# Kernel tuning notes

Measured on AMD Instinct MI355X. Metric: run time of the kernel, lower is better.

The kernel has to match this reference:

```python
import jax, jax.numpy as jnp
import numpy as np

N, C, D = 200000, 100, 256      # samples, classes, dim_out
M = N // C                       # samples per class (y is sorted, equal counts)
K = int(1000 * 0.1)              # num_overlab = int(args.d * args.overlap_ratio)
ALPHA = 1.0                      # args.alpha


def setup_inputs() -> dict:
    key = jax.random.key(0)
    x = jax.random.normal(key, (N, D), dtype=jnp.float32)
    # sorted, balanced labels: class c occupies rows [c*M, (c+1)*M)
    y = jnp.arange(N, dtype=jnp.int32) // M
    return {"x": x, "y": y}


def reference(x, y):
    # per-class means (faithful to get_centers); y is sorted/balanced so a
    # reshape gives the static per-class grouping used below
    xg = x.reshape(C, M, D)                         # [C, M, D]
    centers = jax.ops.segment_sum(x, y, num_segments=C) / M  # [C, D]

    # full center-to-sample L2 distances via ||c||^2 + ||x||^2 - 2 c.x
    x2 = jnp.sum(xg * xg, axis=-1)                  # [C2, M]
    c2 = jnp.sum(centers * centers, axis=-1)        # [C1]
    cx = jnp.einsum('cd,gmd->cgm', centers, xg)     # [C1, C2, M]
    dist = jnp.sqrt(jnp.maximum(c2[:, None, None] + x2[None, :, :] - 2.0 * cx, 0.0))

    # positive: K largest distances from each center to its own samples
    pos = jnp.einsum('iim->im', dist)               # diagonal blocks [C, M]
    pos_mean = jax.lax.top_k(pos, K)[0].mean(axis=1)            # [C]

    # negative: K smallest distances from center c1 to samples of class c2
    neg_mean = (-jax.lax.top_k(-dist, K)[0]).mean(axis=-1)      # [C1, C2]

    lo = jnp.maximum(ALPHA + pos_mean[:, None] - neg_mean, 0.0)  # [C1, C2]
    mask = 1.0 - jnp.eye(C, dtype=lo.dtype)         # skip class_type2 == class_type1
    loss = jnp.sum(lo * mask) / ((C + 1) * (C / 2))
    return loss.reshape(1)
```

## Files before the change

### kernel.cpp

```cpp
#include <hip/hip_runtime.h>
#include <hip/hip_fp16.h>
#include <math.h>

#define N_S 200000
#define C_CLS 100
#define D_DIM 256
#define M_PER 2000
#define K_SEL 100
#define EP_STRIDE 136

typedef __attribute__((ext_vector_type(8))) short short8;
typedef __attribute__((ext_vector_type(4))) float float4v;

__device__ __forceinline__ unsigned int f2bf(float f){
    unsigned int u = __float_as_uint(f);
    u += 0x7FFFu + ((u >> 16) & 1u);
    return u >> 16;
}

__global__ __launch_bounds__(256) void k_sums(const float* __restrict__ x,
                                              float* __restrict__ partial){
    int c = blockIdx.x, s = blockIdx.y;
    int t = threadIdx.x, w = t >> 6, ch = t & 63;
    int rbase = c * M_PER + s * 125;
    float a0 = 0.f, a1 = 0.f, a2 = 0.f, a3 = 0.f;
    for (int i = 0; i < 32; ++i){
        int rl = w + 4 * i;
        if (rl < 125){
            float4v v = *(const float4v*)(x + (size_t)(rbase + rl) * D_DIM + ch * 4);
            a0 += v[0]; a1 += v[1]; a2 += v[2]; a3 += v[3];
        }
    }
    float4v o = {a0, a1, a2, a3};
    *(float4v*)(partial + ((size_t)((c * 16 + s) * 4 + w)) * D_DIM + ch * 4) = o;
}

__global__ __launch_bounds__(256) void k_centers(const float* __restrict__ partial,
                                                 unsigned short* __restrict__ cbf,
                                                 float* __restrict__ c2){
    int c = blockIdx.x, d = threadIdx.x;
    const float* pp = partial + (size_t)c * 64 * D_DIM + d;
    float v = 0.f;
    #pragma unroll
    for (int s = 0; s < 64; ++s) v += pp[(size_t)s * D_DIM];
    v *= (1.0f / (float)M_PER);
    cbf[c * D_DIM + d] = (unsigned short)f2bf(v);
    float sq = v * v;
    #pragma unroll
    for (int m = 1; m < 64; m <<= 1) sq += __shfl_xor(sq, m);
    __shared__ float sred[4];
    if ((threadIdx.x & 63) == 0) sred[threadIdx.x >> 6] = sq;
    __syncthreads();
    if (threadIdx.x == 0) c2[c] = (sred[0] + sred[1]) + (sred[2] + sred[3]);
}

__global__ __launch_bounds__(256, 3) void k_gemm(const float* __restrict__ x,
                                                 const unsigned short* __restrict__ cbf,
                                                 const float* __restrict__ c2,
                                                 _Float16* __restrict__ dist2h){
    __shared__ unsigned short s_cent[C_CLS * 264];
    __shared__ float s_c2[C_CLS];
    int tid = threadIdx.x;
    {
        const uint4* g = (const uint4*)cbf;
        #pragma unroll
        for (int i = 0; i < 13; ++i){
            int q = i * 256 + tid;
            if (q < 3200){
                uint4 v = g[q];
                int row = q >> 5;
                int col = q & 31;
                *(uint4*)((char*)s_cent + row * 528 + col * 16) = v;
            }
        }
        if (tid < C_CLS) s_c2[tid] = c2[tid];
    }
    __syncthreads();

    int wid = tid >> 6, lane = tid & 63, lo = lane & 15, hi = lane >> 4;
    int sbase = blockIdx.x * 128 + wid * 32;
    int j0 = sbase + lo, j1 = sbase + 16 + lo;
    int jr0 = j0 < N_S ? j0 : N_S - 1;
    int jr1 = j1 < N_S ? j1 : N_S - 1;

    float4v acc[7][2];
    #pragma unroll
    for (int a = 0; a < 7; ++a){
        #pragma unroll
        for (int b = 0; b < 2; ++b) acc[a][b] = (float4v){0.f, 0.f, 0.f, 0.f};
    }
    float px2_0 = 0.f, px2_1 = 0.f;

    const float* xr0 = x + (size_t)jr0 * D_DIM + hi * 8;
    const float* xr1 = x + (size_t)jr1 * D_DIM + hi * 8;
    for (int ks = 0; ks < 8; ++ks){
        int k0 = ks * 32;
        float4v v0 = *(const float4v*)(xr0 + k0);
        float4v v1 = *(const float4v*)(xr0 + k0 + 4);
        float4v w0 = *(const float4v*)(xr1 + k0);
        float4v w1 = *(const float4v*)(xr1 + k0 + 4);
        px2_0 += v0[0]*v0[0] + v0[1]*v0[1] + v0[2]*v0[2] + v0[3]*v0[3]
               + v1[0]*v1[0] + v1[1]*v1[1] + v1[2]*v1[2] + v1[3]*v1[3];
        px2_1 += w0[0]*w0[0] + w0[1]*w0[1] + w0[2]*w0[2] + w0[3]*w0[3]
               + w1[0]*w1[0] + w1[1]*w1[1] + w1[2]*w1[2] + w1[3]*w1[3];
        short8 bfr0, bfr1;
        bfr0[0]=(short)f2bf(v0[0]); bfr0[1]=(short)f2bf(v0[1]); bfr0[2]=(short)f2bf(v0[2]); bfr0[3]=(short)f2bf(v0[3]);
        bfr0[4]=(short)f2bf(v1[0]); bfr0[5]=(short)f2bf(v1[1]); bfr0[6]=(short)f2bf(v1[2]); bfr0[7]=(short)f2bf(v1[3]);
        bfr1[0]=(short)f2bf(w0[0]); bfr1[1]=(short)f2bf(w0[1]); bfr1[2]=(short)f2bf(w0[2]); bfr1[3]=(short)f2bf(w0[3]);
        bfr1[4]=(short)f2bf(w1[0]); bfr1[5]=(short)f2bf(w1[1]); bfr1[6]=(short)f2bf(w1[2]); bfr1[7]=(short)f2bf(w1[3]);
        #pragma unroll
        for (int cf = 0; cf < 7; ++cf){
            short8 afr = *(const short8*)((const char*)s_cent + (cf*16 + lo) * 528 + (k0 + hi*8) * 2);
            acc[cf][0] = __builtin_amdgcn_mfma_f32_16x16x32_bf16(afr, bfr0, acc[cf][0], 0, 0, 0);
            acc[cf][1] = __builtin_amdgcn_mfma_f32_16x16x32_bf16(afr, bfr1, acc[cf][1], 0, 0, 0);
        }
    }

    px2_0 += __shfl_xor(px2_0, 16); px2_0 += __shfl_xor(px2_0, 32);
    px2_1 += __shfl_xor(px2_1, 16); px2_1 += __shfl_xor(px2_1, 32);

    __syncthreads();
    _Float16* ep = (_Float16*)s_cent;
    #pragma unroll
    for (int sf = 0; sf < 2; ++sf){
        float x2 = sf ? px2_1 : px2_0;
        int lj = wid * 32 + sf * 16 + lo;
        #pragma unroll
        for (int cf = 0; cf < 7; ++cf){
            #pragma unroll
            for (int r = 0; r < 4; ++r){
                int c1 = cf * 16 + hi * 4 + r;
                if (c1 < C_CLS){
                    float d2 = s_c2[c1] + x2 - 2.0f * acc[cf][sf][r];
                    ep[c1 * EP_STRIDE + lj] = (_Float16)fmaxf(d2, 0.f);
                }
            }
        }
    }
    __syncthreads();

    int blockbase = blockIdx.x * 128;
    int vj = N_S - blockbase; vj = vj > 128 ? 128 : vj;
    for (int q = tid; q < C_CLS * 16; q += 256){
        int row = q >> 4, st = (q & 15) * 8;
        if (st < vj){
            uint4 v = *(const uint4*)(ep + row * EP_STRIDE + st);
            *(uint4*)(dist2h + (size_t)row * N_S + blockbase + st) = v;
        }
    }
}

__global__ __launch_bounds__(256) void k_select(const _Float16* __restrict__ dist2h,
                                                float* __restrict__ pos_mean,
                                                float* __restrict__ neg_mean){
    int lane = threadIdx.x & 63;
    int pair = blockIdx.x * 4 + (threadIdx.x >> 6);
    int c1 = pair / 100, c2 = pair - c1 * 100;
    bool diag = (c1 == c2);
    const uint4* base =
        (const uint4*)(dist2h + (size_t)c1 * N_S + (size_t)c2 * M_PER);

    int keys[32];
    int kmin = 0x10000, kmax = 0;
    #pragma unroll
    for (int i = 0; i < 4; ++i){
        int q = i * 64 + lane;
        if (q < 250){
            uint4 v = base[q];
            unsigned wds[4] = {v.x, v.y, v.z, v.w};
            #pragma unroll
            for (int j = 0; j < 4; ++j){
                int klo = (int)(wds[j] & 0xFFFFu);
                int khi = (int)(wds[j] >> 16);
                if (diag){ klo = 0xFFFF - klo; khi = 0xFFFF - khi; }
                keys[i*8 + 2*j]     = klo;
                keys[i*8 + 2*j + 1] = khi;
                kmin = klo < kmin ? klo : kmin;  kmin = khi < kmin ? khi : kmin;
                kmax = klo > kmax ? klo : kmax;  kmax = khi > kmax ? khi : kmax;
            }
        } else {
            #pragma unroll
            for (int j = 0; j < 8; ++j) keys[i*8 + j] = 0x10000;
        }
    }
    #pragma unroll
    for (int m = 1; m < 64; m <<= 1){
        int a = __shfl_xor(kmin, m); kmin = a < kmin ? a : kmin;
        int b = __shfl_xor(kmax, m); kmax = b > kmax ? b : kmax;
    }

    int lo = kmin, hi = kmax;
    while (lo < hi){
        int mid = (lo + hi) >> 1;
        int c = 0;
        #pragma unroll
        for (int i = 0; i < 32; ++i) c += (keys[i] <= mid) ? 1 : 0;
        #pragma unroll
        for (int m = 1; m < 64; m <<= 1) c += __shfl_xor(c, m);
        if (c >= K_SEL) hi = mid; else lo = mid + 1;
    }
    int t = lo;

    float sb = 0.f;
    int nb = 0;
    #pragma unroll
    for (int i = 0; i < 32; ++i){
        int key = keys[i];
        if (key < t){
            unsigned short u = (unsigned short)(diag ? (0xFFFF - key) : key);
            sb += sqrtf(__half2float(__ushort_as_half(u)));
            nb++;
        }
    }
    #pragma unroll
    for (int m = 1; m < 64; m <<= 1){
        sb += __shfl_xor(sb, m);
        nb += __shfl_xor(nb, m);
    }
    if (lane == 0){
        unsigned short ut = (unsigned short)(diag ? (0xFFFF - t) : t);
        float tval = sqrtf(__half2float(__ushort_as_half(ut)));
        int need = K_SEL - nb;
        float mean = (sb + (float)need * tval) * (1.0f / (float)K_SEL);
        if (diag) pos_mean[c1] = mean; else neg_mean[pair] = mean;
    }
}

__global__ __launch_bounds__(256) void k_loss(const float* __restrict__ pos_mean,
                                              const float* __restrict__ neg_mean,
                                              float* __restrict__ out){
    __shared__ float sred[4];
    int tid = threadIdx.x;
    float s = 0.f;
    for (int idx = tid; idx < C_CLS * C_CLS; idx += 256){
        int c1 = idx / 100, c2 = idx - c1 * 100;
        if (c1 != c2){
            float v = 1.0f + pos_mean[c1] - neg_mean[idx];
            s += fmaxf(v, 0.f);
        }
    }
    #pragma unroll
    for (int m = 1; m < 64; m <<= 1) s += __shfl_xor(s, m);
    if ((tid & 63) == 0) sred[tid >> 6] = s;
    __syncthreads();
    if (tid == 0) out[0] = ((sred[0] + sred[1]) + (sred[2] + sred[3])) * (1.0f / 5050.0f);
}

extern "C" void kernel_launch(void* const* d_in, const int* in_sizes, int n_in,
                              void* d_out, int out_size, void* d_ws, size_t ws_size,
                              hipStream_t stream){
    const float* x = (const float*)d_in[0];
    char* ws = (char*)d_ws;
    _Float16*       dist2h   = (_Float16*)(ws);
    float*          partial  = (float*)(ws + 40000000);
    unsigned short* cbf      = (unsigned short*)(ws + 46553600);
    float*          c2       = (float*)(ws + 46604800);
    float*          pos_mean = (float*)(ws + 46605200);
    float*          neg_mean = (float*)(ws + 46605600);
    float* out = (float*)d_out;

    hipLaunchKernelGGL(k_sums,    dim3(100, 16), dim3(256), 0, stream, x, partial);
    hipLaunchKernelGGL(k_centers, dim3(C_CLS),   dim3(256), 0, stream, partial, cbf, c2);
    hipLaunchKernelGGL(k_gemm,    dim3(1563),    dim3(256), 0, stream, x, cbf, c2, dist2h);
    hipLaunchKernelGGL(k_select,  dim3(2500),    dim3(256), 0, stream, dist2h, pos_mean, neg_mean);
    hipLaunchKernelGGL(k_loss,    dim3(1),       dim3(256), 0, stream, pos_mean, neg_mean, out);
}
```

Baseline: 127.3 us.

## Fuse select and loss via ticket, prefetch GEMM inputs, reduce partial sums in-block

Several changes at once. k_sums now combines its four wave partials in shared memory, so k_centers reads 16 rows instead of 64. k_gemm issues the x loads for the next k-step before the MFMAs of the current one, so global load latency overlaps the matrix math. k_select uses ballot/popcount counting instead of shuffle reductions, and the final loss is folded into it with an atomic ticket: the last block to finish computes the loss, which removes the separate k_loss launch but adds a memset launch.

```diff
diff --git a/kernel.cpp b/kernel.cpp
--- a/kernel.cpp
+++ b/kernel.cpp
@@ -8,6 +8,7 @@
 #define M_PER 2000
 #define K_SEL 100
 #define EP_STRIDE 136
+#define NPAIR_BLOCKS 2500
 
 typedef __attribute__((ext_vector_type(8))) short short8;
 typedef __attribute__((ext_vector_type(4))) float float4v;
@@ -20,6 +21,7 @@
 
 __global__ __launch_bounds__(256) void k_sums(const float* __restrict__ x,
                                               float* __restrict__ partial){
+    __shared__ float4v sred[4][64];
     int c = blockIdx.x, s = blockIdx.y;
     int t = threadIdx.x, w = t >> 6, ch = t & 63;
     int rbase = c * M_PER + s * 125;
@@ -31,18 +33,24 @@
             a0 += v[0]; a1 += v[1]; a2 += v[2]; a3 += v[3];
         }
     }
-    float4v o = {a0, a1, a2, a3};
-    *(float4v*)(partial + ((size_t)((c * 16 + s) * 4 + w)) * D_DIM + ch * 4) = o;
+    sred[w][ch] = (float4v){a0, a1, a2, a3};
+    __syncthreads();
+    if (t < 64){
+        float4v r0 = sred[0][t], r1 = sred[1][t], r2 = sred[2][t], r3 = sred[3][t];
+        float4v o = {(r0[0]+r1[0])+(r2[0]+r3[0]), (r0[1]+r1[1])+(r2[1]+r3[1]),
+                     (r0[2]+r1[2])+(r2[2]+r3[2]), (r0[3]+r1[3])+(r2[3]+r3[3])};
+        *(float4v*)(partial + (size_t)(c * 16 + s) * D_DIM + t * 4) = o;
+    }
 }
 
 __global__ __launch_bounds__(256) void k_centers(const float* __restrict__ partial,
                                                  unsigned short* __restrict__ cbf,
                                                  float* __restrict__ c2){
     int c = blockIdx.x, d = threadIdx.x;
-    const float* pp = partial + (size_t)c * 64 * D_DIM + d;
+    const float* pp = partial + (size_t)c * 16 * D_DIM + d;
     float v = 0.f;
     #pragma unroll
-    for (int s = 0; s < 64; ++s) v += pp[(size_t)s * D_DIM];
+    for (int s = 0; s < 16; ++s) v += pp[(size_t)s * D_DIM];
     v *= (1.0f / (float)M_PER);
     cbf[c * D_DIM + d] = (unsigned short)f2bf(v);
     float sq = v * v;
@@ -61,6 +69,19 @@
     __shared__ unsigned short s_cent[C_CLS * 264];
     __shared__ float s_c2[C_CLS];
     int tid = threadIdx.x;
+    int wid = tid >> 6, lane = tid & 63, lo = lane & 15, hi = lane >> 4;
+    int sbase = blockIdx.x * 128 + wid * 32;
+    int j0 = sbase + lo, j1 = sbase + 16 + lo;
+    int jr0 = j0 < N_S ? j0 : N_S - 1;
+    int jr1 = j1 < N_S ? j1 : N_S - 1;
+    const float* xr0 = x + (size_t)jr0 * D_DIM + hi * 8;
+    const float* xr1 = x + (size_t)jr1 * D_DIM + hi * 8;
+
+    float4v cv0 = *(const float4v*)(xr0);
+    float4v cv1 = *(const float4v*)(xr0 + 4);
+    float4v cw0 = *(const float4v*)(xr1);
+    float4v cw1 = *(const float4v*)(xr1 + 4);
+
     {
         const uint4* g = (const uint4*)cbf;
         #pragma unroll
@@ -77,12 +98,6 @@
     }
     __syncthreads();
 
-    int wid = tid >> 6, lane = tid & 63, lo = lane & 15, hi = lane >> 4;
-    int sbase = blockIdx.x * 128 + wid * 32;
-    int j0 = sbase + lo, j1 = sbase + 16 + lo;
-    int jr0 = j0 < N_S ? j0 : N_S - 1;
-    int jr1 = j1 < N_S ? j1 : N_S - 1;
-
     float4v acc[7][2];
     #pragma unroll
     for (int a = 0; a < 7; ++a){
@@ -91,29 +106,32 @@
     }
     float px2_0 = 0.f, px2_1 = 0.f;
 
-    const float* xr0 = x + (size_t)jr0 * D_DIM + hi * 8;
-    const float* xr1 = x + (size_t)jr1 * D_DIM + hi * 8;
     for (int ks = 0; ks < 8; ++ks){
+        float4v nv0, nv1, nw0, nw1;
+        if (ks < 7){
+            int kn = (ks + 1) * 32;
+            nv0 = *(const float4v*)(xr0 + kn);
+            nv1 = *(const float4v*)(xr0 + kn + 4);
+            nw0 = *(const float4v*)(xr1 + kn);
+            nw1 = *(const float4v*)(xr1 + kn + 4);
+        }
         int k0 = ks * 32;
-        float4v v0 = *(const float4v*)(xr0 + k0);
-        float4v v1 = *(const float4v*)(xr0 + k0 + 4);
-        float4v w0 = *(const float4v*)(xr1 + k0);
-        float4v w1 = *(const float4v*)(xr1 + k0 + 4);
-        px2_0 += v0[0]*v0[0] + v0[1]*v0[1] + v0[2]*v0[2] + v0[3]*v0[3]
-               + v1[0]*v1[0] + v1[1]*v1[1] + v1[2]*v1[2] + v1[3]*v1[3];
-        px2_1 += w0[0]*w0[0] + w0[1]*w0[1] + w0[2]*w0[2] + w0[3]*w0[3]
-               + w1[0]*w1[0] + w1[1]*w1[1] + w1[2]*w1[2] + w1[3]*w1[3];
+        px2_0 += cv0[0]*cv0[0] + cv0[1]*cv0[1] + cv0[2]*cv0[2] + cv0[3]*cv0[3]
+               + cv1[0]*cv1[0] + cv1[1]*cv1[1] + cv1[2]*cv1[2] + cv1[3]*cv1[3];
+        px2_1 += cw0[0]*cw0[0] + cw0[1]*cw0[1] + cw0[2]*cw0[2] + cw0[3]*cw0[3]
+               + cw1[0]*cw1[0] + cw1[1]*cw1[1] + cw1[2]*cw1[2] + cw1[3]*cw1[3];
         short8 bfr0, bfr1;
-        bfr0[0]=(short)f2bf(v0[0]); bfr0[1]=(short)f2bf(v0[1]); bfr0[2]=(short)f2bf(v0[2]); bfr0[3]=(short)f2bf(v0[3]);
-        bfr0[4]=(short)f2bf(v1[0]); bfr0[5]=(short)f2bf(v1[1]); bfr0[6]=(short)f2bf(v1[2]); bfr0[7]=(short)f2bf(v1[3]);
-        bfr1[0]=(short)f2bf(w0[0]); bfr1[1]=(short)f2bf(w0[1]); bfr1[2]=(short)f2bf(w0[2]); bfr1[3]=(short)f2bf(w0[3]);
-        bfr1[4]=(short)f2bf(w1[0]); bfr1[5]=(short)f2bf(w1[1]); bfr1[6]=(short)f2bf(w1[2]); bfr1[7]=(short)f2bf(w1[3]);
+        bfr0[0]=(short)f2bf(cv0[0]); bfr0[1]=(short)f2bf(cv0[1]); bfr0[2]=(short)f2bf(cv0[2]); bfr0[3]=(short)f2bf(cv0[3]);
+        bfr0[4]=(short)f2bf(cv1[0]); bfr0[5]=(short)f2bf(cv1[1]); bfr0[6]=(short)f2bf(cv1[2]); bfr0[7]=(short)f2bf(cv1[3]);
+        bfr1[0]=(short)f2bf(cw0[0]); bfr1[1]=(short)f2bf(cw0[1]); bfr1[2]=(short)f2bf(cw0[2]); bfr1[3]=(short)f2bf(cw0[3]);
+        bfr1[4]=(short)f2bf(cw1[0]); bfr1[5]=(short)f2bf(cw1[1]); bfr1[6]=(short)f2bf(cw1[2]); bfr1[7]=(short)f2bf(cw1[3]);
         #pragma unroll
         for (int cf = 0; cf < 7; ++cf){
             short8 afr = *(const short8*)((const char*)s_cent + (cf*16 + lo) * 528 + (k0 + hi*8) * 2);
             acc[cf][0] = __builtin_amdgcn_mfma_f32_16x16x32_bf16(afr, bfr0, acc[cf][0], 0, 0, 0);
             acc[cf][1] = __builtin_amdgcn_mfma_f32_16x16x32_bf16(afr, bfr1, acc[cf][1], 0, 0, 0);
         }
+        cv0 = nv0; cv1 = nv1; cw0 = nw0; cw1 = nw1;
     }
 
     px2_0 += __shfl_xor(px2_0, 16); px2_0 += __shfl_xor(px2_0, 32);
@@ -150,11 +168,14 @@
     }
 }
 
-__global__ __launch_bounds__(256) void k_select(const _Float16* __restrict__ dist2h,
-                                                float* __restrict__ pos_mean,
-                                                float* __restrict__ neg_mean){
-    int lane = threadIdx.x & 63;
-    int pair = blockIdx.x * 4 + (threadIdx.x >> 6);
+__global__ __launch_bounds__(256) void k_selloss(const _Float16* __restrict__ dist2h,
+                                                 float* __restrict__ pos_mean,
+                                                 float* __restrict__ neg_mean,
+                                                 unsigned* __restrict__ ticket,
+                                                 float* __restrict__ out){
+    int tid = threadIdx.x;
+    int lane = tid & 63;
+    int pair = blockIdx.x * 4 + (tid >> 6);
     int c1 = pair / 100, c2 = pair - c1 * 100;
     bool diag = (c1 == c2);
     const uint4* base =
@@ -194,9 +215,8 @@
         int mid = (lo + hi) >> 1;
         int c = 0;
         #pragma unroll
-        for (int i = 0; i < 32; ++i) c += (keys[i] <= mid) ? 1 : 0;
-        #pragma unroll
-        for (int m = 1; m < 64; m <<= 1) c += __shfl_xor(c, m);
+        for (int i = 0; i < 32; ++i)
+            c += (int)__popcll(__ballot(keys[i] <= mid));
         if (c >= K_SEL) hi = mid; else lo = mid + 1;
     }
     int t = lo;
@@ -213,37 +233,50 @@
         }
     }
     #pragma unroll
-    for (int m = 1; m < 64; m <<= 1){
-        sb += __shfl_xor(sb, m);
-        nb += __shfl_xor(nb, m);
+    for (int m = 1; m < 64; m <<= 1) sb += __shfl_xor(sb, m);
+    nb = (int)__popcll(__ballot(0 != 0));
+    {
+        int cnt = 0;
+        #pragma unroll
+        for (int i = 0; i < 32; ++i)
+            cnt += (int)__popcll(__ballot(keys[i] < t));
+        nb = cnt;
     }
     if (lane == 0){
         unsigned short ut = (unsigned short)(diag ? (0xFFFF - t) : t);
         float tval = sqrtf(__half2float(__ushort_as_half(ut)));
         int need = K_SEL - nb;
         float mean = (sb + (float)need * tval) * (1.0f / (float)K_SEL);
-        if (diag) pos_mean[c1] = mean; else neg_mean[pair] = mean;
-    }
-}
-
-__global__ __launch_bounds__(256) void k_loss(const float* __restrict__ pos_mean,
-                                              const float* __restrict__ neg_mean,
-                                              float* __restrict__ out){
-    __shared__ float sred[4];
-    int tid = threadIdx.x;
+        if (diag)
+            __hip_atomic_store(&pos_mean[c1], mean, __ATOMIC_RELAXED, __HIP_MEMORY_SCOPE_AGENT);
+        else
+            __hip_atomic_store(&neg_mean[pair], mean, __ATOMIC_RELAXED, __HIP_MEMORY_SCOPE_AGENT);
+    }
+    __syncthreads();
+
+    __shared__ int isLast;
+    if (tid == 0){
+        unsigned old = __hip_atomic_fetch_add(ticket, 1u, __ATOMIC_ACQ_REL, __HIP_MEMORY_SCOPE_AGENT);
+        isLast = (old == (unsigned)(NPAIR_BLOCKS - 1));
+    }
+    __syncthreads();
+    if (!isLast) return;
+
     float s = 0.f;
     for (int idx = tid; idx < C_CLS * C_CLS; idx += 256){
-        int c1 = idx / 100, c2 = idx - c1 * 100;
-        if (c1 != c2){
-            float v = 1.0f + pos_mean[c1] - neg_mean[idx];
-            s += fmaxf(v, 0.f);
+        int a = idx / 100, b = idx - a * 100;
+        if (a != b){
+            float pm = __hip_atomic_load(&pos_mean[a], __ATOMIC_RELAXED, __HIP_MEMORY_SCOPE_AGENT);
+            float nm = __hip_atomic_load(&neg_mean[idx], __ATOMIC_RELAXED, __HIP_MEMORY_SCOPE_AGENT);
+            s += fmaxf(1.0f + pm - nm, 0.f);
         }
     }
     #pragma unroll
     for (int m = 1; m < 64; m <<= 1) s += __shfl_xor(s, m);
-    if ((tid & 63) == 0) sred[tid >> 6] = s;
-    __syncthreads();
-    if (tid == 0) out[0] = ((sred[0] + sred[1]) + (sred[2] + sred[3])) * (1.0f / 5050.0f);
+    __shared__ float lred[4];
+    if ((tid & 63) == 0) lred[tid >> 6] = s;
+    __syncthreads();
+    if (tid == 0) out[0] = ((lred[0] + lred[1]) + (lred[2] + lred[3])) * (1.0f / 5050.0f);
 }
 
 extern "C" void kernel_launch(void* const* d_in, const int* in_sizes, int n_in,
@@ -253,15 +286,17 @@
     char* ws = (char*)d_ws;
     _Float16*       dist2h   = (_Float16*)(ws);
     float*          partial  = (float*)(ws + 40000000);
-    unsigned short* cbf      = (unsigned short*)(ws + 46553600);
-    float*          c2       = (float*)(ws + 46604800);
-    float*          pos_mean = (float*)(ws + 46605200);
-    float*          neg_mean = (float*)(ws + 46605600);
+    unsigned short* cbf      = (unsigned short*)(ws + 41638400);
+    float*          c2       = (float*)(ws + 41689600);
+    float*          pos_mean = (float*)(ws + 41690000);
+    float*          neg_mean = (float*)(ws + 41690400);
+    unsigned*       ticket   = (unsigned*)(ws + 41730400);
     float* out = (float*)d_out;
 
-    hipLaunchKernelGGL(k_sums,    dim3(100, 16), dim3(256), 0, stream, x, partial);
-    hipLaunchKernelGGL(k_centers, dim3(C_CLS),   dim3(256), 0, stream, partial, cbf, c2);
-    hipLaunchKernelGGL(k_gemm,    dim3(1563),    dim3(256), 0, stream, x, cbf, c2, dist2h);
-    hipLaunchKernelGGL(k_select,  dim3(2500),    dim3(256), 0, stream, dist2h, pos_mean, neg_mean);
-    hipLaunchKernelGGL(k_loss,    dim3(1),       dim3(256), 0, stream, pos_mean, neg_mean, out);
-}
+    hipMemsetAsync(ticket, 0, sizeof(unsigned), stream);
+    hipLaunchKernelGGL(k_sums,    dim3(100, 16),       dim3(256), 0, stream, x, partial);
+    hipLaunchKernelGGL(k_centers, dim3(C_CLS),         dim3(256), 0, stream, partial, cbf, c2);
+    hipLaunchKernelGGL(k_gemm,    dim3(1563),          dim3(256), 0, stream, x, cbf, c2, dist2h);
+    hipLaunchKernelGGL(k_selloss, dim3(NPAIR_BLOCKS),  dim3(256), 0, stream,
+                       dist2h, pos_mean, neg_mean, ticket, out);
+}
```

Result: slower. 162.6 us (+27.7%).
